# Performance work log

Measured on AMD Instinct MI355X. Metric: run time of the kernel, lower is better.

The kernel has to match this reference:

```python
import jax, jax.numpy as jnp
import numpy as np

NUM_HEADS = 16


def setup_inputs() -> dict:
    key = jax.random.key(0)
    ks = jax.random.split(key, 9)
    B, N, C, R, T = 16, 1024, 1024, 64, 10
    s = 0.02
    x = jax.random.normal(ks[0], (B, N, C), dtype=jnp.float32)
    W_qkv = jax.random.normal(ks[1], (3 * C, C), dtype=jnp.float32) * s
    W_proj = jax.random.normal(ks[2], (C, C), dtype=jnp.float32) * s
    b_proj = jax.random.normal(ks[3], (C,), dtype=jnp.float32) * s
    A_k = jax.random.normal(ks[4], (T, R, C), dtype=jnp.float32) * s
    B_k = jax.random.normal(ks[5], (T, C, R), dtype=jnp.float32) * s
    A_v = jax.random.normal(ks[6], (T, R, C), dtype=jnp.float32) * s
    B_v = jax.random.normal(ks[7], (T, C, R), dtype=jnp.float32) * s
    return {"x": x, "W_qkv": W_qkv, "W_proj": W_proj, "b_proj": b_proj,
            "A_k": A_k, "B_k": B_k, "A_v": A_v, "B_v": B_v, "task": 4}


def reference(x, W_qkv, W_proj, b_proj, A_k, B_k, A_v, B_v, task):
    B, N, C = x.shape
    H = NUM_HEADS
    hd = C // H
    scale = hd ** (-0.5)

    # qkv projection: x @ W_qkv.T -> [B,N,3C] -> [3,B,H,N,hd]
    qkv = (x @ W_qkv.T).reshape(B, N, 3, H, hd).transpose(2, 0, 3, 1, 4)
    q, k, v = qkv[0], qkv[1], qkv[2]

    # merged LoRA weights: sum_{t<=task} B[t] @ A[t] -> [C, C]
    w_k = jnp.einsum('tcr,trd->cd', B_k[:task + 1], A_k[:task + 1])
    w_v = jnp.einsum('tcr,trd->cd', B_v[:task + 1], A_v[:task + 1])
    # F.linear(x, W) = x @ W.T ; reshape to [B,H,N,hd]
    dk = (x @ w_k.T).reshape(B, N, H, hd).transpose(0, 2, 1, 3)
    dv = (x @ w_v.T).reshape(B, N, H, hd).transpose(0, 2, 1, 3)
    k = k + dk
    v = v + dv

    attn = jax.nn.softmax(jnp.einsum('bhnd,bhmd->bhnm', q, k) * scale, axis=-1)
    out = jnp.einsum('bhnm,bhmd->bhnd', attn, v)
    out = out.transpose(0, 2, 1, 3).reshape(B, N, C)
    return out @ W_proj.T + b_proj
```

## Files before the change

### kernel.cpp

```cpp
#include <hip/hip_runtime.h>

typedef __attribute__((ext_vector_type(4))) float f32x4;
typedef __attribute__((ext_vector_type(8))) short s16x8;
typedef __attribute__((ext_vector_type(2))) unsigned int u32x2;
typedef __attribute__((ext_vector_type(4))) unsigned int u32x4;

#define LOG2E 1.44269504088896340736f

__device__ inline unsigned short f2b(float f) {
  unsigned int u = __float_as_uint(f);
  unsigned int r = (u + 0x7FFFu + ((u >> 16) & 1u)) >> 16;
  return (unsigned short)r;
}

__device__ inline unsigned int cvtpk_bf16(float lo, float hi) {
  unsigned int r;
  asm("v_cvt_pk_bf16_f32 %0, %1, %2" : "=v"(r) : "v"(lo), "v"(hi));
  return r;
}

__device__ inline void gload_lds16(const unsigned short* g, unsigned short* l) {
  __builtin_amdgcn_global_load_lds(
      (const __attribute__((address_space(1))) unsigned int*)g,
      (__attribute__((address_space(3))) unsigned int*)l, 16, 0, 0);
}

__global__ __launch_bounds__(256) void lora_merge(const float* __restrict__ A_,
                                                  const float* __restrict__ B_,
                                                  float* __restrict__ Wd,
                                                  const int* __restrict__ taskp) {
  __shared__ float Bs[64][65];
  __shared__ float As[64][65];
  const int tile = blockIdx.x;
  const int c0 = (tile >> 4) * 64, d0 = (tile & 15) * 64;
  const int tid = threadIdx.x;
  const int tx = tid & 15, ty = tid >> 4;
  const int T = *taskp + 1;
  float acc[4][4] = {};
  const int r = tid >> 2, cb = (tid & 3) * 16;
  for (int t = 0; t < T; ++t) {
    __syncthreads();
    const float* srcB = B_ + (size_t)t * 65536 + (size_t)(c0 + r) * 64 + cb;
    const float* srcA = A_ + (size_t)t * 65536 + (size_t)r * 1024 + d0 + cb;
#pragma unroll
    for (int j = 0; j < 16; j += 4) {
      f32x4 vb = *(const f32x4*)(srcB + j);
      Bs[r][cb + j] = vb.x; Bs[r][cb + j + 1] = vb.y;
      Bs[r][cb + j + 2] = vb.z; Bs[r][cb + j + 3] = vb.w;
      f32x4 va = *(const f32x4*)(srcA + j);
      As[r][cb + j] = va.x; As[r][cb + j + 1] = va.y;
      As[r][cb + j + 2] = va.z; As[r][cb + j + 3] = va.w;
    }
    __syncthreads();
#pragma unroll 8
    for (int rr = 0; rr < 64; ++rr) {
      float bv[4], av[4];
#pragma unroll
      for (int i = 0; i < 4; ++i) bv[i] = Bs[ty * 4 + i][rr];
#pragma unroll
      for (int j = 0; j < 4; ++j) av[j] = As[rr][tx * 4 + j];
#pragma unroll
      for (int i = 0; i < 4; ++i)
#pragma unroll
        for (int j = 0; j < 4; ++j) acc[i][j] += bv[i] * av[j];
    }
  }
#pragma unroll
  for (int i = 0; i < 4; ++i)
#pragma unroll
    for (int j = 0; j < 4; ++j)
      Wd[(size_t)(c0 + ty * 4 + i) * 1024 + d0 + tx * 4 + j] = acc[i][j];
}

__global__ void cvt_bf16(const float* __restrict__ in, unsigned short* __restrict__ out, int n4) {
  int i = blockIdx.x * 256 + threadIdx.x;
  if (i >= n4) return;
  f32x4 v = ((const f32x4*)in)[i];
  unsigned short o0 = f2b(v.x), o1 = f2b(v.y), o2 = f2b(v.z), o3 = f2b(v.w);
  unsigned long long pack = (unsigned long long)o0 | ((unsigned long long)o1 << 16) |
                            ((unsigned long long)o2 << 32) | ((unsigned long long)o3 << 48);
  ((unsigned long long*)out)[i] = pack;
}

__global__ void build_wc(const float* __restrict__ Wqkv, const float* __restrict__ wk,
                         const float* __restrict__ wv, unsigned short* __restrict__ Wc) {
  int i = blockIdx.x * 256 + threadIdx.x;
  int e = i * 4;
  f32x4 v = *(const f32x4*)(Wqkv + e);
  int row = e >> 10;
  if (row >= 2048) {
    f32x4 d = *(const f32x4*)(wv + (e - 2097152));
    v = v + d;
  } else if (row >= 1024) {
    f32x4 d = *(const f32x4*)(wk + (e - 1048576));
    v = v + d;
  }
  unsigned short o0 = f2b(v.x), o1 = f2b(v.y), o2 = f2b(v.z), o3 = f2b(v.w);
  unsigned long long pack = (unsigned long long)o0 | ((unsigned long long)o1 << 16) |
                            ((unsigned long long)o2 << 32) | ((unsigned long long)o3 << 48);
  ((unsigned long long*)Wc)[i] = pack;
}

template <int OUT_BF16, int ADD_BIAS>
__global__ __launch_bounds__(512, 1) void gemm256(const unsigned short* __restrict__ A,
                                                  const unsigned short* __restrict__ B,
                                                  void* __restrict__ Cout,
                                                  const float* __restrict__ bias,
                                                  int M, int N, int K) {
  __shared__ unsigned short SA[4][8192];
  __shared__ unsigned short SB[4][8192];
  const int tid = threadIdx.x;
  const int w = tid >> 6, l = tid & 63;
  const int lr = l & 15, lg = l >> 4;
  const int wm = w >> 2, wn = w & 3;
  const int bx = blockIdx.x, by = blockIdx.y;

  const int cs = tid ^ (((tid >> 5) & 1) << 1);
  const int r_st = ((cs >> 6) << 4) | ((cs >> 2) & 15);
  const int k_st = (cs & 3) << 3;
  const unsigned short* gA0 = A + (size_t)(by * 256 + r_st) * K + k_st;
  const unsigned short* gA1 = A + (size_t)(by * 256 + 128 + r_st) * K + k_st;
  const unsigned short* gB0 = B + (size_t)(bx * 256 + r_st) * K + k_st;
  const unsigned short* gB1 = B + (size_t)(bx * 256 + 128 + r_st) * K + k_st;
  const int wb = w * 512;

  const int swz = ((lr >> 3) & 1) << 4;
  const int fbase = lr * 32 + lg * 8;
  const int hA = wm * 4096;
  const int hB = (wn >> 1) * 4096;
  const int nb = (wn & 1) * 4;

  f32x4 acc[8][4] = {};
  const int NT = K >> 5;

#pragma unroll
  for (int t = 0; t < 2; ++t) {
    gload_lds16(gA0 + t * 32, &SA[t][wb]);
    gload_lds16(gA1 + t * 32, &SA[t][4096 + wb]);
    gload_lds16(gB0 + t * 32, &SB[t][wb]);
    gload_lds16(gB1 + t * 32, &SB[t][4096 + wb]);
  }
  asm volatile("s_waitcnt vmcnt(4)" ::: "memory");
  __builtin_amdgcn_s_barrier();
  __builtin_amdgcn_sched_barrier(0);

  for (int t = 0; t < NT; ++t) {
    const int slot = t & 3;
    const int ts = (t + 2 < NT) ? (t + 2) : (NT - 1);
    const int ssl = (t + 2) & 3;
    const unsigned short* sa = &SA[slot][hA];
    const unsigned short* sb = &SB[slot][hB];
    s16x8 af[8], bf[2];
#pragma unroll
    for (int m = 0; m < 8; ++m)
      af[m] = *(const s16x8*)&sa[(m * 512 + fbase) ^ swz];
#pragma unroll
    for (int n = 0; n < 2; ++n)
      bf[n] = *(const s16x8*)&sb[((nb + n) * 512 + fbase) ^ swz];
    gload_lds16(gA0 + ts * 32, &SA[ssl][wb]);
    gload_lds16(gA1 + ts * 32, &SA[ssl][4096 + wb]);
    __builtin_amdgcn_s_barrier();
    asm volatile("s_waitcnt lgkmcnt(0)" ::: "memory");
    __builtin_amdgcn_sched_barrier(0);
    __builtin_amdgcn_s_setprio(1);
#pragma unroll
    for (int m = 0; m < 8; ++m)
#pragma unroll
      for (int n = 0; n < 2; ++n)
        acc[m][n] = __builtin_amdgcn_mfma_f32_16x16x32_bf16(af[m], bf[n], acc[m][n], 0, 0, 0);
    __builtin_amdgcn_s_setprio(0);
    __builtin_amdgcn_sched_barrier(0);
    __builtin_amdgcn_s_barrier();
#pragma unroll
    for (int n = 0; n < 2; ++n)
      bf[n] = *(const s16x8*)&sb[((nb + 2 + n) * 512 + fbase) ^ swz];
    gload_lds16(gB0 + ts * 32, &SB[ssl][wb]);
    gload_lds16(gB1 + ts * 32, &SB[ssl][4096 + wb]);
    __builtin_amdgcn_s_barrier();
    asm volatile("s_waitcnt lgkmcnt(0)" ::: "memory");
    __builtin_amdgcn_sched_barrier(0);
    __builtin_amdgcn_s_setprio(1);
#pragma unroll
    for (int m = 0; m < 8; ++m)
#pragma unroll
      for (int n = 0; n < 2; ++n)
        acc[m][2 + n] = __builtin_amdgcn_mfma_f32_16x16x32_bf16(af[m], bf[n], acc[m][2 + n], 0, 0, 0);
    __builtin_amdgcn_s_setprio(0);
    __builtin_amdgcn_sched_barrier(0);
    asm volatile("s_waitcnt vmcnt(4)" ::: "memory");
    __builtin_amdgcn_s_barrier();
    __builtin_amdgcn_sched_barrier(0);
  }

  const int crow0 = by * 256 + wm * 128;
  const int ccol0 = bx * 256 + wn * 64;
  if (OUT_BF16) {
    unsigned short* C = (unsigned short*)Cout;
#pragma unroll
    for (int m = 0; m < 8; ++m)
#pragma unroll
      for (int n = 0; n < 4; ++n)
#pragma unroll
        for (int rr = 0; rr < 4; ++rr) {
          int row = crow0 + m * 16 + lg * 4 + rr;
          int col = ccol0 + n * 16 + lr;
          C[(size_t)row * N + col] = f2b(acc[m][n][rr]);
        }
  } else {
    float* C = (float*)Cout;
#pragma unroll
    for (int m = 0; m < 8; ++m)
#pragma unroll
      for (int n = 0; n < 4; ++n)
#pragma unroll
        for (int rr = 0; rr < 4; ++rr) {
          int row = crow0 + m * 16 + lg * 4 + rr;
          int col = ccol0 + n * 16 + lr;
          float b = ADD_BIAS ? bias[col] : 0.f;
          C[(size_t)row * N + col] = acc[m][n][rr] + b;
        }
  }
}

__global__ __launch_bounds__(64) void transpose_v(const unsigned short* __restrict__ qkv,
                                                  unsigned short* __restrict__ vT) {
  __shared__ unsigned short T[64 * 65];
  const int bh = blockIdx.x >> 4;
  const int nt = blockIdx.x & 15;
  const int b = bh >> 4, h = bh & 15;
  const int l = threadIdx.x;
  const unsigned short* src = qkv + (size_t)(b * 1024 + nt * 64) * 3072 + 2048 + h * 64;
#pragma unroll
  for (int p = 0; p < 8; ++p) {
    int slot = p * 64 + l;
    int n = slot >> 3, dc = (slot & 7) * 8;
    u32x4 v = *(const u32x4*)(src + (size_t)n * 3072 + dc);
    const unsigned short* vs = (const unsigned short*)&v;
#pragma unroll
    for (int j = 0; j < 8; ++j) T[n * 65 + dc + j] = vs[j];
  }
  __syncthreads();
  unsigned short* dst = vT + (size_t)bh * 65536 + nt * 64;
#pragma unroll
  for (int p = 0; p < 8; ++p) {
    int slot = p * 64 + l;
    int d = slot >> 3, nc = (slot & 7) * 8;
    union { unsigned short s[8]; u32x4 v; } tmp;
#pragma unroll
    for (int j = 0; j < 8; ++j) tmp.s[j] = T[(nc + j) * 65 + d];
    *(u32x4*)(dst + (size_t)d * 1024 + nc) = tmp.v;
  }
}

__global__ __launch_bounds__(512) void attn_fwd(const unsigned short* __restrict__ qkv,
                                                const unsigned short* __restrict__ vT,
                                                unsigned short* __restrict__ out) {
  const int tid = threadIdx.x;
  const int w = tid >> 6, l = tid & 63;
  const int lr = l & 15, lg = l >> 4;
  const int bid = blockIdx.x;
  const int g = ((bid >> 6) << 3) | (bid & 7);
  const int qt = (bid >> 3) & 7;
  const int b = g >> 4, h = g & 15;

  __shared__ unsigned short Ks[2][4096];
  __shared__ unsigned short Vs[2][4096];
  __shared__ unsigned int Ps[8][576];

  const size_t base = (size_t)b * 1024 * 3072 + h * 64;
  const unsigned short* Qp = qkv + base;
  const unsigned short* Kp = qkv + base + 1024;
  const unsigned short* vTp = vT + (size_t)(b * 16 + h) * 65536;

  const float SSCALE = 0.125f * LOG2E;
  const int qrow = qt * 128 + w * 16 + lr;
  s16x8 qf[2];
  qf[0] = *(const s16x8*)(Qp + (size_t)qrow * 3072 + lg * 8);
  qf[1] = *(const s16x8*)(Qp + (size_t)qrow * 3072 + 32 + lg * 8);
#pragma unroll
  for (int kk = 0; kk < 2; ++kk)
#pragma unroll
    for (int j = 0; j < 8; ++j) {
      float f = __uint_as_float(((unsigned int)(unsigned short)qf[kk][j]) << 16) * SSCALE;
      qf[kk][j] = (short)f2b(f);
    }

  f32x4 o[4] = {};
  float lrun = 0.f;

  const int srow = tid >> 3;
  const int csrc = (tid & 7) ^ (srow & 7);

  gload_lds16(Kp + (size_t)srow * 3072 + csrc * 8, &Ks[0][w * 512]);
  gload_lds16(vTp + (size_t)srow * 1024 + csrc * 8, &Vs[0][w * 512]);
  __syncthreads();

  for (int t = 0; t < 16; ++t) {
    const int cur = t & 1;
    if (t < 15) {
      const int kv1 = (t + 1) * 64;
      gload_lds16(Kp + (size_t)(kv1 + srow) * 3072 + csrc * 8, &Ks[cur ^ 1][w * 512]);
      gload_lds16(vTp + (size_t)srow * 1024 + kv1 + csrc * 8, &Vs[cur ^ 1][w * 512]);
    }
    const unsigned short* Kb = &Ks[cur][0];
    const unsigned short* Vb = &Vs[cur][0];

    f32x4 sc[4];
#pragma unroll
    for (int tt = 0; tt < 4; ++tt) {
      f32x4 a = {0.f, 0.f, 0.f, 0.f};
#pragma unroll
      for (int kk = 0; kk < 2; ++kk) {
        int krow = tt * 16 + lr;
        s16x8 kf = *(const s16x8*)&Kb[krow * 64 + ((((kk * 32 + lg * 8) >> 3) ^ (krow & 7)) << 3)];
        a = __builtin_amdgcn_mfma_f32_16x16x32_bf16(kf, qf[kk], a, 0, 0, 0);
      }
      sc[tt] = a;
    }

#pragma unroll
    for (int tt = 0; tt < 4; ++tt) {
      float p0 = exp2f(sc[tt][0]);
      float p1 = exp2f(sc[tt][1]);
      float p2 = exp2f(sc[tt][2]);
      float p3 = exp2f(sc[tt][3]);
      lrun += (p0 + p1) + (p2 + p3);
      u32x2 pk;
      pk.x = cvtpk_bf16(p0, p1);
      pk.y = cvtpk_bf16(p2, p3);
      *(u32x2*)&Ps[w][lr * 36 + tt * 8 + lg * 2] = pk;
    }
    __builtin_amdgcn_sched_barrier(0);

#pragma unroll
    for (int kk = 0; kk < 2; ++kk) {
      u32x4 pu = *(const u32x4*)&Ps[w][lr * 36 + kk * 16 + lg * 4];
      s16x8 pf = __builtin_bit_cast(s16x8, pu);
#pragma unroll
      for (int dt = 0; dt < 4; ++dt) {
        int vrow = dt * 16 + lr;
        s16x8 vf = *(const s16x8*)&Vb[vrow * 64 + ((((kk * 32 + lg * 8) >> 3) ^ (vrow & 7)) << 3)];
        o[dt] = __builtin_amdgcn_mfma_f32_16x16x32_bf16(pf, vf, o[dt], 0, 0, 0);
      }
    }
    __syncthreads();
  }

  lrun += __shfl_xor(lrun, 16);
  lrun += __shfl_xor(lrun, 32);
  float lq[4];
#pragma unroll
  for (int rr = 0; rr < 4; ++rr) lq[rr] = 1.f / __shfl(lrun, lg * 4 + rr);

  const size_t orow0 = (size_t)b * 1024 + qt * 128 + w * 16;
#pragma unroll
  for (int dt = 0; dt < 4; ++dt)
#pragma unroll
    for (int rr = 0; rr < 4; ++rr)
      out[(orow0 + lg * 4 + rr) * 1024 + h * 64 + dt * 16 + lr] = f2b(o[dt][rr] * lq[rr]);
}

extern "C" void kernel_launch(void* const* d_in, const int* in_sizes, int n_in,
                              void* d_out, int out_size, void* d_ws, size_t ws_size,
                              hipStream_t stream) {
  const float* x = (const float*)d_in[0];
  const float* Wqkv = (const float*)d_in[1];
  const float* Wproj = (const float*)d_in[2];
  const float* bproj = (const float*)d_in[3];
  const float* A_k = (const float*)d_in[4];
  const float* B_k = (const float*)d_in[5];
  const float* A_v = (const float*)d_in[6];
  const float* B_v = (const float*)d_in[7];
  const int* task = (const int*)d_in[8];

  char* ws = (char*)d_ws;
  float* wk = (float*)ws;
  float* wv = (float*)(ws + (4ull << 20));
  unsigned short* xb = (unsigned short*)(ws + (8ull << 20));
  unsigned short* Wc = (unsigned short*)(ws + (40ull << 20));
  unsigned short* Wp = (unsigned short*)(ws + (46ull << 20));
  unsigned short* qkv = (unsigned short*)(ws + (48ull << 20));
  unsigned short* ao = (unsigned short*)(ws + (144ull << 20));
  unsigned short* vT = xb;

  lora_merge<<<256, 256, 0, stream>>>(A_k, B_k, wk, task);
  lora_merge<<<256, 256, 0, stream>>>(A_v, B_v, wv, task);
  cvt_bf16<<<16384, 256, 0, stream>>>(x, xb, 4194304);
  cvt_bf16<<<1024, 256, 0, stream>>>(Wproj, Wp, 262144);
  build_wc<<<3072, 256, 0, stream>>>(Wqkv, wk, wv, Wc);
  gemm256<1, 0><<<dim3(12, 64), 512, 0, stream>>>(xb, Wc, qkv, nullptr, 16384, 3072, 1024);
  transpose_v<<<4096, 64, 0, stream>>>(qkv, vT);
  attn_fwd<<<2048, 512, 0, stream>>>(qkv, vT, ao);
  gemm256<0, 1><<<dim3(4, 64), 512, 0, stream>>>(ao, Wp, d_out, bproj, 16384, 1024, 1024);
}
```

Measured before the change: 350.9 us.

## Merge prep kernels, deepen GEMM prefetch, and remap GEMM blocks across XCDs

The two LoRA-merge launches become one launch with a 2D grid, and the two bf16 conversion launches become one, cutting launch overhead. The GEMM now prefetches three K-tiles ahead instead of two within its 4-slot LDS ring, with the vmcnt waits adjusted to match, to hide more global-load latency. GEMM block indices are also permuted so that consecutive tiles land on the same XCD (8-way interleave), which should improve L2 reuse. The deeper prefetch risks a slot-reuse hazard if the barriers do not fully guard the slot being overwritten.

```diff
diff --git a/kernel.cpp b/kernel.cpp
--- a/kernel.cpp
+++ b/kernel.cpp
@@ -25,10 +25,16 @@
       (__attribute__((address_space(3))) unsigned int*)l, 16, 0, 0);
 }
 
-__global__ __launch_bounds__(256) void lora_merge(const float* __restrict__ A_,
-                                                  const float* __restrict__ B_,
-                                                  float* __restrict__ Wd,
+__global__ __launch_bounds__(256) void lora_merge(const float* __restrict__ A_k,
+                                                  const float* __restrict__ B_k,
+                                                  const float* __restrict__ A_v,
+                                                  const float* __restrict__ B_v,
+                                                  float* __restrict__ wk,
+                                                  float* __restrict__ wv,
                                                   const int* __restrict__ taskp) {
+  const float* A_ = blockIdx.y ? A_v : A_k;
+  const float* B_ = blockIdx.y ? B_v : B_k;
+  float* Wd = blockIdx.y ? wv : wk;
   __shared__ float Bs[64][65];
   __shared__ float As[64][65];
   const int tile = blockIdx.x;
@@ -72,14 +78,19 @@
       Wd[(size_t)(c0 + ty * 4 + i) * 1024 + d0 + tx * 4 + j] = acc[i][j];
 }
 
-__global__ void cvt_bf16(const float* __restrict__ in, unsigned short* __restrict__ out, int n4) {
+__global__ void prep_cvt(const float* __restrict__ x, const float* __restrict__ Wproj,
+                         unsigned short* __restrict__ xb, unsigned short* __restrict__ Wp) {
   int i = blockIdx.x * 256 + threadIdx.x;
-  if (i >= n4) return;
-  f32x4 v = ((const f32x4*)in)[i];
+  const float* src;
+  unsigned short* dst;
+  int idx;
+  if (i < 4194304) { src = x; dst = xb; idx = i; }
+  else { idx = i - 4194304; if (idx >= 262144) return; src = Wproj; dst = Wp; }
+  f32x4 v = ((const f32x4*)src)[idx];
   unsigned short o0 = f2b(v.x), o1 = f2b(v.y), o2 = f2b(v.z), o3 = f2b(v.w);
   unsigned long long pack = (unsigned long long)o0 | ((unsigned long long)o1 << 16) |
                             ((unsigned long long)o2 << 32) | ((unsigned long long)o3 << 48);
-  ((unsigned long long*)out)[i] = pack;
+  ((unsigned long long*)dst)[idx] = pack;
 }
 
 __global__ void build_wc(const float* __restrict__ Wqkv, const float* __restrict__ wk,
@@ -113,7 +124,11 @@
   const int w = tid >> 6, l = tid & 63;
   const int lr = l & 15, lg = l >> 4;
   const int wm = w >> 2, wn = w & 3;
-  const int bx = blockIdx.x, by = blockIdx.y;
+
+  const int lin = blockIdx.y * gridDim.x + blockIdx.x;
+  const int cpx = (gridDim.x * gridDim.y) >> 3;
+  const int s = (lin & 7) * cpx + (lin >> 3);
+  const int bx = s % gridDim.x, by = s / gridDim.x;
 
   const int cs = tid ^ (((tid >> 5) & 1) << 1);
   const int r_st = ((cs >> 6) << 4) | ((cs >> 2) & 15);
@@ -134,20 +149,20 @@
   const int NT = K >> 5;
 
 #pragma unroll
-  for (int t = 0; t < 2; ++t) {
+  for (int t = 0; t < 3; ++t) {
     gload_lds16(gA0 + t * 32, &SA[t][wb]);
     gload_lds16(gA1 + t * 32, &SA[t][4096 + wb]);
     gload_lds16(gB0 + t * 32, &SB[t][wb]);
     gload_lds16(gB1 + t * 32, &SB[t][4096 + wb]);
   }
-  asm volatile("s_waitcnt vmcnt(4)" ::: "memory");
+  asm volatile("s_waitcnt vmcnt(8)" ::: "memory");
   __builtin_amdgcn_s_barrier();
   __builtin_amdgcn_sched_barrier(0);
 
   for (int t = 0; t < NT; ++t) {
     const int slot = t & 3;
-    const int ts = (t + 2 < NT) ? (t + 2) : (NT - 1);
-    const int ssl = (t + 2) & 3;
+    const int ts = (t + 3 < NT) ? (t + 3) : (NT - 1);
+    const int ssl = (t + 3) & 3;
     const unsigned short* sa = &SA[slot][hA];
     const unsigned short* sb = &SB[slot][hB];
     s16x8 af[8], bf[2];
@@ -187,7 +202,7 @@
         acc[m][2 + n] = __builtin_amdgcn_mfma_f32_16x16x32_bf16(af[m], bf[n], acc[m][2 + n], 0, 0, 0);
     __builtin_amdgcn_s_setprio(0);
     __builtin_amdgcn_sched_barrier(0);
-    asm volatile("s_waitcnt vmcnt(4)" ::: "memory");
+    asm volatile("s_waitcnt vmcnt(8)" ::: "memory");
     __builtin_amdgcn_s_barrier();
     __builtin_amdgcn_sched_barrier(0);
   }
@@ -383,10 +398,8 @@
   unsigned short* ao = (unsigned short*)(ws + (144ull << 20));
   unsigned short* vT = xb;
 
-  lora_merge<<<256, 256, 0, stream>>>(A_k, B_k, wk, task);
-  lora_merge<<<256, 256, 0, stream>>>(A_v, B_v, wv, task);
-  cvt_bf16<<<16384, 256, 0, stream>>>(x, xb, 4194304);
-  cvt_bf16<<<1024, 256, 0, stream>>>(Wproj, Wp, 262144);
+  lora_merge<<<dim3(256, 2), 256, 0, stream>>>(A_k, B_k, A_v, B_v, wk, wv, task);
+  prep_cvt<<<17408, 256, 0, stream>>>(x, Wproj, xb, Wp);
   build_wc<<<3072, 256, 0, stream>>>(Wqkv, wk, wv, Wc);
   gemm256<1, 0><<<dim3(12, 64), 512, 0, stream>>>(xb, Wc, qkv, nullptr, 16384, 3072, 1024);
   transpose_v<<<4096, 64, 0, stream>>>(qkv, vT);
```

After: 328.4 us. 1.07x faster.
